# Optimization experiments

Measured on AMD Instinct MI355X. Metric: run time of the kernel, lower is better.

## Reference

```python
import jax, jax.numpy as jnp
import numpy as np

B, D, T, H = 2048, 512, 16, 1024   # batch, covariate_dim, treatment_dim, mlp hidden
K, M = 50, 16                       # k_neighbors, manifold_dim


def _mlp(xt, W1, b1, W2, b2):
    # outcome model: [B, D+T] -> [B, 1]
    return jnp.tanh(xt @ W1 + b1) @ W2 + b2


def setup_inputs() -> dict:
    key = jax.random.key(0)
    k0, k1, k2, k3, k4 = jax.random.split(key, 5)
    x = jax.random.normal(k0, (B, D), dtype=jnp.float32)
    t = jax.random.normal(k1, (B, T), dtype=jnp.float32)
    perturbations = jax.random.normal(k2, (B, D), dtype=jnp.float32)
    W1 = jax.random.normal(k3, (D + T, H), dtype=jnp.float32) / np.float32(np.sqrt(D + T))
    b1 = jnp.zeros((H,), dtype=jnp.float32)
    W2 = jax.random.normal(k4, (H, 1), dtype=jnp.float32) / np.float32(np.sqrt(H))
    b2 = jnp.zeros((1,), dtype=jnp.float32)
    return {"x": x, "t": t, "perturbations": perturbations,
            "W1": W1, "b1": b1, "W2": W2, "b2": b2}


def reference(x, t, perturbations, W1, b1, W2, b2):
    # grad of sum(y) w.r.t. x (create_graph analog handled by composing jax.grad)
    def scalar_out(xx):
        return _mlp(jnp.concatenate([xx, t], axis=-1), W1, b1, W2, b2).sum()
    grad_x = jax.grad(scalar_out)(x)                      # [B, D]

    # kNN on perturbations (squared distances preserve topk-smallest ordering)
    sq = jnp.sum(perturbations * perturbations, axis=-1)  # [B]
    d2 = sq[:, None] + sq[None, :] - 2.0 * (perturbations @ perturbations.T)
    _, idx = jax.lax.top_k(-d2, K)                        # [B, K] nearest (incl. self)

    neigh = perturbations[idx]                            # [B, K, D] gather
    centered = neigh - neigh.mean(axis=1, keepdims=True)
    # batched reduced SVD: Vt has shape [B, min(K,D), D]
    _, _, Vt = jnp.linalg.svd(centered, full_matrices=False)
    basis = jnp.swapaxes(Vt[:, :M, :], 1, 2)              # [B, D, M] top-M right sing. vecs

    # projection of grad onto tangent space, summed squared norm
    coef = jnp.einsum('bdm,bd->bm', basis, grad_x)        # [B, M]
    proj = jnp.einsum('bdm,bm->bd', basis, coef)          # [B, D]
    return jnp.sum(proj * proj) / B
```

## Files before the change

kernel.cpp:

```cpp
#include <hip/hip_runtime.h>
#include <math.h>
#include <float.h>

#define B_ 2048
#define D_ 512
#define T_ 16
#define H_ 1024
#define K_ 50
#define M_ 16
#define NSWEEP 1
#define SX_STRIDE 2656
#define SLAB 128
#define SROW 136
#define FS 52

typedef __attribute__((ext_vector_type(8))) short s16x8;
typedef __attribute__((ext_vector_type(4))) float f32x4;

__device__ __forceinline__ float bsum64(float v) {
  #pragma unroll
  for (int o = 1; o < 64; o <<= 1) v += __shfl_xor(v, o);
  return v;
}

__device__ __forceinline__ unsigned bf16_rne(float v) {
  union { float f; unsigned u; } a; a.f = v;
  return (a.u + 0x7FFFu + ((a.u >> 16) & 1u)) >> 16;
}
__device__ __forceinline__ float bf16_val(unsigned h) {
  union { unsigned u; float f; } a; a.u = h << 16;
  return a.f;
}
__device__ __forceinline__ void split_bf16(float v, unsigned short* h, unsigned short* l) {
  unsigned hh = bf16_rne(v);
  *h = (unsigned short)hh;
  *l = (unsigned short)bf16_rne(v - bf16_val(hh));
}

__global__ __launch_bounds__(256)
void prep_rows(const float* __restrict__ x, const float* __restrict__ t,
               const float* __restrict__ P,
               unsigned short* __restrict__ xh, unsigned short* __restrict__ xl,
               unsigned short* __restrict__ ph, unsigned short* __restrict__ pl,
               float* __restrict__ sq) {
  const int b = blockIdx.x, tid = threadIdx.x;
  for (int c = tid; c < 544; c += 256) {
    float v = 0.f;
    if (c < 512) v = x[(size_t)b * 512 + c];
    else if (c < 528) v = t[(size_t)b * 16 + (c - 512)];
    unsigned short hh, ll; split_bf16(v, &hh, &ll);
    xh[(size_t)b * 544 + c] = hh;
    xl[(size_t)b * 544 + c] = ll;
  }
  float s = 0.f;
  for (int c = tid; c < 512; c += 256) {
    float v = P[(size_t)b * 512 + c];
    s += v * v;
    unsigned short hh, ll; split_bf16(v, &hh, &ll);
    ph[(size_t)b * 512 + c] = hh;
    pl[(size_t)b * 512 + c] = ll;
  }
  __shared__ float red[4];
  s = bsum64(s);
  if ((tid & 63) == 0) red[tid >> 6] = s;
  __syncthreads();
  if (tid == 0) sq[b] = (red[0] + red[1]) + (red[2] + red[3]);
}

__global__ __launch_bounds__(256)
void conv_w1(const float* __restrict__ W1,
             unsigned short* __restrict__ th, unsigned short* __restrict__ tl,
             unsigned short* __restrict__ wh, unsigned short* __restrict__ wl) {
  __shared__ float tile[32][33];
  const int tx = threadIdx.x & 31, ty = threadIdx.x >> 5;
  const int kb = blockIdx.x * 32, hb = blockIdx.y * 32;
  #pragma unroll
  for (int j = 0; j < 4; j++) {
    int k = kb + ty + j * 8;
    float v = (k < 528) ? W1[(size_t)k * 1024 + hb + tx] : 0.f;
    tile[ty + j * 8][tx] = v;
    if (k < 528) {
      unsigned short hh, ll; split_bf16(v, &hh, &ll);
      wh[(size_t)k * 1024 + hb + tx] = hh;
      wl[(size_t)k * 1024 + hb + tx] = ll;
    }
  }
  __syncthreads();
  #pragma unroll
  for (int j = 0; j < 4; j++) {
    int hrow = hb + ty + j * 8;
    float v = tile[tx][ty + j * 8];
    unsigned short hh, ll; split_bf16(v, &hh, &ll);
    th[(size_t)hrow * 544 + kb + tx] = hh;
    tl[(size_t)hrow * 544 + kb + tx] = ll;
  }
}

template <int EPI, int PASSES>
__global__ __launch_bounds__(256)
void mfma_nt(const unsigned short* __restrict__ Ah, const unsigned short* __restrict__ Al, int lda,
             const unsigned short* __restrict__ Bh, const unsigned short* __restrict__ Bl, int ldb,
             int K, float* __restrict__ C, int ldc,
             const float* __restrict__ b1, const float* __restrict__ W2,
             unsigned short* __restrict__ acth, unsigned short* __restrict__ actl) {
  __shared__ unsigned short sAh[64 * 40], sBh[64 * 40];
  __shared__ unsigned short sAl[PASSES == 3 ? 64 * 40 : 16];
  __shared__ unsigned short sBl[PASSES == 3 ? 64 * 40 : 16];
  const int tid = threadIdx.x;
  const int lane = tid & 63, wv = tid >> 6;
  const int wm = wv >> 1, wn = wv & 1;
  const int lr = lane & 15, lq = lane >> 4;
  const int m0 = blockIdx.y * 64, n0 = blockIdx.x * 64;
  const int srow = tid >> 2, sk = (tid & 3) * 8;
  f32x4 acc[2][2];
  #pragma unroll
  for (int mt = 0; mt < 2; mt++)
    #pragma unroll
    for (int nt = 0; nt < 2; nt++)
      #pragma unroll
      for (int i = 0; i < 4; i++) acc[mt][nt][i] = 0.f;

  for (int kb = 0; kb < K; kb += 32) {
    float4 va = *(const float4*)(Ah + (size_t)(m0 + srow) * lda + kb + sk);
    float4 vc = *(const float4*)(Bh + (size_t)(n0 + srow) * ldb + kb + sk);
    float4 vb, vd;
    if (PASSES == 3) {
      vb = *(const float4*)(Al + (size_t)(m0 + srow) * lda + kb + sk);
      vd = *(const float4*)(Bl + (size_t)(n0 + srow) * ldb + kb + sk);
    }
    __syncthreads();
    *(float4*)&sAh[srow * 40 + sk] = va;
    *(float4*)&sBh[srow * 40 + sk] = vc;
    if (PASSES == 3) {
      *(float4*)&sAl[srow * 40 + sk] = vb;
      *(float4*)&sBl[srow * 40 + sk] = vd;
    }
    __syncthreads();
    s16x8 fah[2], fal[2], fbh[2], fbl[2];
    #pragma unroll
    for (int mt = 0; mt < 2; mt++) {
      const int r = wm * 32 + mt * 16 + lr;
      fah[mt] = *(const s16x8*)&sAh[r * 40 + lq * 8];
      if (PASSES == 3) fal[mt] = *(const s16x8*)&sAl[r * 40 + lq * 8];
    }
    #pragma unroll
    for (int nt = 0; nt < 2; nt++) {
      const int r = wn * 32 + nt * 16 + lr;
      fbh[nt] = *(const s16x8*)&sBh[r * 40 + lq * 8];
      if (PASSES == 3) fbl[nt] = *(const s16x8*)&sBl[r * 40 + lq * 8];
    }
    #pragma unroll
    for (int mt = 0; mt < 2; mt++)
      #pragma unroll
      for (int nt = 0; nt < 2; nt++)
        acc[mt][nt] = __builtin_amdgcn_mfma_f32_16x16x32_bf16(fah[mt], fbh[nt], acc[mt][nt], 0, 0, 0);
    if (PASSES == 3) {
      #pragma unroll
      for (int mt = 0; mt < 2; mt++)
        #pragma unroll
        for (int nt = 0; nt < 2; nt++)
          acc[mt][nt] = __builtin_amdgcn_mfma_f32_16x16x32_bf16(fah[mt], fbl[nt], acc[mt][nt], 0, 0, 0);
      #pragma unroll
      for (int mt = 0; mt < 2; mt++)
        #pragma unroll
        for (int nt = 0; nt < 2; nt++)
          acc[mt][nt] = __builtin_amdgcn_mfma_f32_16x16x32_bf16(fal[mt], fbh[nt], acc[mt][nt], 0, 0, 0);
    }
  }

  #pragma unroll
  for (int nt = 0; nt < 2; nt++) {
    const int n = n0 + wn * 32 + nt * 16 + lr;
    float bb = 0.f, ww = 0.f;
    if (EPI == 1) { bb = b1[n]; ww = W2[n]; }
    #pragma unroll
    for (int mt = 0; mt < 2; mt++) {
      #pragma unroll
      for (int r = 0; r < 4; r++) {
        const int m = m0 + wm * 32 + mt * 16 + lq * 4 + r;
        float v = acc[mt][nt][r];
        if (EPI == 0) {
          C[(size_t)m * ldc + n] = v;
        } else if (EPI == 1) {
          float z = v + bb;
          float e = __builtin_amdgcn_exp2f(fabsf(z) * -2.885390082f);
          float rc = __builtin_amdgcn_rcpf(1.f + e);
          float s = 4.f * e * rc * rc * ww;
          unsigned short hh, ll; split_bf16(s, &hh, &ll);
          acth[(size_t)m * ldc + n] = hh;
          actl[(size_t)m * ldc + n] = ll;
        } else {
          unsigned short hh, ll; split_bf16(v, &hh, &ll);
          acth[(size_t)m * ldc + n] = hh;
          actl[(size_t)m * ldc + n] = ll;
        }
      }
    }
  }
}

__global__ __launch_bounds__(256)
void sbuild_kernel(const unsigned short* __restrict__ ph, const unsigned short* __restrict__ pl,
                   const unsigned short* __restrict__ gh, const unsigned short* __restrict__ gl,
                   const int* __restrict__ idx, float* __restrict__ Sx) {
  __shared__ unsigned short sh[64 * SROW];
  __shared__ unsigned short sl[64 * SROW];
  __shared__ int ids[K_];
  const int b = blockIdx.x;
  const int tid = threadIdx.x;
  if (tid < K_) ids[tid] = idx[b * K_ + tid];
  const int lane = tid & 63, wv = tid >> 6;
  const int wm = wv >> 1, wn = wv & 1;
  const int lr = lane & 15, lq = lane >> 4;
  const int strow = tid >> 4, stk = (tid & 15) * 8;
  __syncthreads();

  f32x4 acc[2][2];
  #pragma unroll
  for (int mt = 0; mt < 2; mt++)
    #pragma unroll
    for (int nt = 0; nt < 2; nt++)
      #pragma unroll
      for (int i = 0; i < 4; i++) acc[mt][nt][i] = 0.f;

  for (int kb = 0; kb < 512; kb += SLAB) {
    __syncthreads();
    #pragma unroll
    for (int p = 0; p < 4; p++) {
      const int r = p * 16 + strow;
      if (r < 51) {
        const unsigned short* srch = (r < 50) ? ph + (size_t)ids[r] * 512 : gh + (size_t)b * 512;
        const unsigned short* srcl = (r < 50) ? pl + (size_t)ids[r] * 512 : gl + (size_t)b * 512;
        *(float4*)&sh[r * SROW + stk] = *(const float4*)(srch + kb + stk);
        *(float4*)&sl[r * SROW + stk] = *(const float4*)(srcl + kb + stk);
      }
    }
    __syncthreads();
    #pragma unroll
    for (int kk = 0; kk < SLAB; kk += 32) {
      s16x8 fah[2], fal[2], fbh[2], fbl[2];
      #pragma unroll
      for (int mt = 0; mt < 2; mt++) {
        const int r = wm * 32 + mt * 16 + lr;
        fah[mt] = *(const s16x8*)&sh[r * SROW + kk + lq * 8];
        fal[mt] = *(const s16x8*)&sl[r * SROW + kk + lq * 8];
      }
      #pragma unroll
      for (int nt = 0; nt < 2; nt++) {
        const int r = wn * 32 + nt * 16 + lr;
        fbh[nt] = *(const s16x8*)&sh[r * SROW + kk + lq * 8];
        fbl[nt] = *(const s16x8*)&sl[r * SROW + kk + lq * 8];
      }
      #pragma unroll
      for (int mt = 0; mt < 2; mt++)
        #pragma unroll
        for (int nt = 0; nt < 2; nt++)
          acc[mt][nt] = __builtin_amdgcn_mfma_f32_16x16x32_bf16(fah[mt], fbh[nt], acc[mt][nt], 0, 0, 0);
      #pragma unroll
      for (int mt = 0; mt < 2; mt++)
        #pragma unroll
        for (int nt = 0; nt < 2; nt++)
          acc[mt][nt] = __builtin_amdgcn_mfma_f32_16x16x32_bf16(fah[mt], fbl[nt], acc[mt][nt], 0, 0, 0);
      #pragma unroll
      for (int mt = 0; mt < 2; mt++)
        #pragma unroll
        for (int nt = 0; nt < 2; nt++)
          acc[mt][nt] = __builtin_amdgcn_mfma_f32_16x16x32_bf16(fal[mt], fbh[nt], acc[mt][nt], 0, 0, 0);
    }
  }

  float* Sb = Sx + (size_t)b * SX_STRIDE;
  #pragma unroll
  for (int nt = 0; nt < 2; nt++) {
    const int n = wn * 32 + nt * 16 + lr;
    #pragma unroll
    for (int mt = 0; mt < 2; mt++) {
      #pragma unroll
      for (int r = 0; r < 4; r++) {
        const int m = wm * 32 + mt * 16 + lq * 4 + r;
        if (m < 51 && n < 52) Sb[m * 52 + n] = acc[mt][nt][r];
      }
    }
  }
}

__device__ __forceinline__ unsigned fkey(float f) {
  unsigned u = __float_as_uint(f);
  return u ^ ((unsigned)((int)u >> 31) | 0x80000000u);
}

__global__ __launch_bounds__(64)
void topk_kernel(const float* __restrict__ G, const float* __restrict__ sq,
                 int* __restrict__ idx) {
  const int b = blockIdx.x, lane = threadIdx.x;
  const float* row = G + (size_t)b * 2048;
  unsigned k[32];
  #pragma unroll
  for (int i = 0; i < 32; i++) {
    const int j = i * 64 + lane;
    k[i] = fkey(sq[j] - 2.f * row[j]);
  }
  unsigned V = 0;
  bool exact = false;
  for (int bit = 31; bit >= 0; bit--) {
    const unsigned cand = V | (1u << bit);
    int cnt = 0;
    #pragma unroll
    for (int i = 0; i < 32; i++) cnt += (k[i] < cand) ? 1 : 0;
    #pragma unroll
    for (int o = 1; o < 64; o <<= 1) cnt += __shfl_xor(cnt, o);
    if (cnt == K_) { V = cand; exact = true; break; }
    if (cnt < K_ + 1) V = cand;
  }
  int base = 0;
  #pragma unroll
  for (int i = 0; i < 32; i++) {
    const bool p = (k[i] < V);
    const unsigned long long mask = __ballot(p);
    if (p) {
      const int pos = base + __popcll(mask & ((1ull << lane) - 1ull));
      idx[b * K_ + pos] = i * 64 + lane;
    }
    base += __popcll(mask);
  }
  if (!exact && base < K_) {
    #pragma unroll
    for (int i = 0; i < 32; i++) {
      if (base >= K_) break;
      const bool p = (k[i] == V);
      const unsigned long long mask = __ballot(p);
      if (p) {
        const int pos = base + __popcll(mask & ((1ull << lane) - 1ull));
        if (pos < K_) idx[b * K_ + pos] = i * 64 + lane;
      }
      base += __popcll(mask);
    }
  }
}

__global__ __launch_bounds__(64, 2)
void final_kernel(const float* __restrict__ Sx, float* __restrict__ out) {
  __shared__ float cols[64 * FS];
  const int b = blockIdx.x;
  const int lane = threadIdx.x;
  const float* Sb = Sx + (size_t)b * SX_STRIDE;

  float q = (lane < K_) ? Sb[50 * 52 + lane] : 0.f;
  float qm = bsum64(q) * (1.f / K_);
  float w = (lane < K_) ? (q - qm) : 0.f;

  float f[K_];
  #pragma unroll
  for (int r = 0; r < K_; r++)
    f[r] = (lane < K_) ? Sb[r * 52 + lane] : 0.f;

  float cm = 0.f;
  #pragma unroll
  for (int r = 0; r < K_; r++) cm += f[r];
  cm *= (1.f / K_);
  float gs = bsum64(lane < K_ ? cm : 0.f) * (1.f / K_);
  float cs = cm - gs;
  #pragma unroll
  for (int r = 0; r < K_; r++) {
    float rm = __shfl(cm, r);
    if (lane < K_) f[r] -= rm + cs;
  }

  float nrm = 0.f;
  #pragma unroll
  for (int r = 0; r < K_; r++) nrm += f[r] * f[r];

  float* my = &cols[lane * FS];
  #pragma unroll
  for (int k = 0; k < 12; k++) {
    float4 t = {f[4 * k], f[4 * k + 1], f[4 * k + 2], f[4 * k + 3]};
    *(float4*)&my[4 * k] = t;
  }
  {
    float4 t = {f[48], f[49], nrm, w};
    *(float4*)&my[48] = t;
  }

  for (int sweep = 0; sweep < NSWEEP; sweep++) {
    for (int r = 0; r < 49; r++) {
      const int kk = (25 * r) % 49;
      int m;
      if (lane >= K_)      m = lane;
      else if (lane == 49) m = kk;
      else if (lane == kk) m = 49;
      else { m = (r - lane) % 49; if (m < 0) m += 49; }

      const float* pc = &cols[m * FS];
      float y[52];
      #pragma unroll
      for (int k = 0; k < 13; k++) {
        float4 t = *(const float4*)&pc[4 * k];
        y[4 * k] = t.x; y[4 * k + 1] = t.y; y[4 * k + 2] = t.z; y[4 * k + 3] = t.w;
      }
      float onrm = y[50];
      float yw   = y[51];

      float d0 = 0.f, d1 = 0.f, d2 = 0.f, d3 = 0.f;
      #pragma unroll
      for (int r2 = 0; r2 < 48; r2 += 4) {
        d0 += f[r2] * y[r2];
        d1 += f[r2 + 1] * y[r2 + 1];
        d2 += f[r2 + 2] * y[r2 + 2];
        d3 += f[r2 + 3] * y[r2 + 3];
      }
      d0 += f[48] * y[48];
      d1 += f[49] * y[49];
      float dot = (d0 + d1) + (d2 + d3);

      const bool isp = lane < m;
      float alpha = isp ? nrm : onrm;
      float beta  = isp ? onrm : nrm;
      float tau = (beta - alpha) * 0.5f * __builtin_amdgcn_rcpf(dot);
      float sg = (tau >= 0.f) ? 1.f : -1.f;
      float s1 = __builtin_amdgcn_sqrtf(1.f + tau * tau);
      float tt = sg * __builtin_amdgcn_rcpf(fabsf(tau) + s1);
      float cc = __builtin_amdgcn_rsqf(1.f + tt * tt);
      float ssv = tt * cc;
      float sr = isp ? -ssv : ssv;
      if (lane >= K_ || fabsf(dot) < 1e-20f) { cc = 1.f; sr = 0.f; }
      #pragma unroll
      for (int r2 = 0; r2 < K_; r2++) f[r2] = cc * f[r2] + sr * y[r2];
      w = cc * w + sr * yw;
      nrm = cc * cc * nrm + sr * sr * onrm + 2.f * cc * sr * dot;

      #pragma unroll
      for (int k = 0; k < 12; k++) {
        float4 t = {f[4 * k], f[4 * k + 1], f[4 * k + 2], f[4 * k + 3]};
        *(float4*)&my[4 * k] = t;
      }
      float4 t = {f[48], f[49], nrm, w};
      *(float4*)&my[48] = t;
    }
  }

  float n2 = 0.f;
  #pragma unroll
  for (int r2 = 0; r2 < K_; r2++) n2 += f[r2] * f[r2];
  int rank = 0;
  #pragma unroll
  for (int j = 0; j < K_; j++) {
    float vj = __shfl(n2, j);
    rank += (vj > n2 || (vj == n2 && j < lane)) ? 1 : 0;
  }
  float lam = sqrtf(n2);
  float contrib = (lane < K_ && rank < M_) ? (w * w / lam) : 0.f;
  contrib = bsum64(contrib);
  if (lane == 0) atomicAdd(out, contrib * (1.f / B_));
}

extern "C" void kernel_launch(void* const* d_in, const int* in_sizes, int n_in,
                              void* d_out, int out_size, void* d_ws, size_t ws_size,
                              hipStream_t stream) {
  const float* x  = (const float*)d_in[0];
  const float* t  = (const float*)d_in[1];
  const float* P  = (const float*)d_in[2];
  const float* W1 = (const float*)d_in[3];
  const float* b1 = (const float*)d_in[4];
  const float* W2 = (const float*)d_in[5];
  float* out = (float*)d_out;

  float* G    = (float*)d_ws;
  float* Sx   = (float*)d_ws;
  unsigned short* xt_h  = (unsigned short*)(G + (size_t)B_ * B_);
  unsigned short* xt_l  = xt_h  + (size_t)B_ * 544;
  unsigned short* w1t_h = xt_l  + (size_t)B_ * 544;
  unsigned short* w1t_l = w1t_h + (size_t)H_ * 544;
  unsigned short* w1_h  = w1t_l + (size_t)H_ * 544;
  unsigned short* w1_l  = w1_h  + (size_t)528 * H_;
  unsigned short* p_h   = w1_l  + (size_t)528 * H_;
  unsigned short* p_l   = p_h   + (size_t)B_ * D_;
  unsigned short* act_h = p_l   + (size_t)B_ * D_;
  unsigned short* act_l = act_h + (size_t)B_ * H_;
  unsigned short* g_h   = act_l + (size_t)B_ * H_;
  unsigned short* g_l   = g_h   + (size_t)B_ * D_;
  float* sq   = (float*)(g_l + (size_t)B_ * D_);
  int*   idx  = (int*)(sq + B_);

  hipMemsetAsync(d_out, 0, sizeof(float), stream);

  prep_rows<<<B_, 256, 0, stream>>>(x, t, P, xt_h, xt_l, p_h, p_l, sq);
  conv_w1<<<dim3(17, 32), 256, 0, stream>>>(W1, w1t_h, w1t_l, w1_h, w1_l);

  mfma_nt<1, 3><<<dim3(H_ / 64, B_ / 64), 256, 0, stream>>>(
      xt_h, xt_l, 544, w1t_h, w1t_l, 544, 544,
      nullptr, H_, b1, W2, act_h, act_l);
  mfma_nt<2, 3><<<dim3(D_ / 64, B_ / 64), 256, 0, stream>>>(
      act_h, act_l, H_, w1_h, w1_l, H_, H_,
      nullptr, D_, nullptr, nullptr, g_h, g_l);
  mfma_nt<0, 1><<<dim3(B_ / 64, B_ / 64), 256, 0, stream>>>(
      p_h, nullptr, D_, p_h, nullptr, D_, D_,
      G, B_, nullptr, nullptr, nullptr, nullptr);

  topk_kernel<<<B_, 64, 0, stream>>>(G, sq, idx);
  sbuild_kernel<<<B_, 256, 0, stream>>>(p_h, p_l, g_h, g_l, idx, Sx);
  final_kernel<<<B_, 64, 0, stream>>>(Sx, out);
}
```

Measured before the change: 257.9 us.

## Split-K the grad GEMM across two slices and sort top-k indices by distance

The second GEMM (activations times W1) is now split along K into two halves via blockIdx.z. Each half writes fp32 partials to workspace, and a new reduce kernel sums them and splits the result into bf16 hi/lo. This doubles the block count from 256 to 512 so more compute units are busy, at the cost of an extra kernel launch and an fp32 round trip through memory. The top-k kernel also now ranks the selected neighbours by key and index before writing, giving a deterministic sorted order for later stages at a small extra cost per row.

```diff
diff --git a/kernel.cpp b/kernel.cpp
--- a/kernel.cpp
+++ b/kernel.cpp
@@ -106,6 +106,12 @@
   __shared__ unsigned short sAh[64 * 40], sBh[64 * 40];
   __shared__ unsigned short sAl[PASSES == 3 ? 64 * 40 : 16];
   __shared__ unsigned short sBl[PASSES == 3 ? 64 * 40 : 16];
+  if (EPI == 3) {
+    const size_t ko = (size_t)blockIdx.z * K;
+    Ah += ko; Bh += ko;
+    if (PASSES == 3) { Al += ko; Bl += ko; }
+    C += (size_t)blockIdx.z * (size_t)(gridDim.y * 64) * ldc;
+  }
   const int tid = threadIdx.x;
   const int lane = tid & 63, wv = tid >> 6;
   const int wm = wv >> 1, wn = wv & 1;
@@ -179,7 +185,7 @@
       for (int r = 0; r < 4; r++) {
         const int m = m0 + wm * 32 + mt * 16 + lq * 4 + r;
         float v = acc[mt][nt][r];
-        if (EPI == 0) {
+        if (EPI == 0 || EPI == 3) {
           C[(size_t)m * ldc + n] = v;
         } else if (EPI == 1) {
           float z = v + bb;
@@ -197,6 +203,15 @@
       }
     }
   }
+}
+
+__global__ __launch_bounds__(256)
+void grad_reduce(const float* __restrict__ Cp,
+                 unsigned short* __restrict__ gh, unsigned short* __restrict__ gl) {
+  const int i = blockIdx.x * 256 + threadIdx.x;
+  float v = Cp[i] + Cp[(size_t)B_ * D_ + i];
+  unsigned short hh, ll; split_bf16(v, &hh, &ll);
+  gh[i] = hh; gl[i] = ll;
 }
 
 __global__ __launch_bounds__(256)
@@ -292,6 +307,8 @@
 __global__ __launch_bounds__(64)
 void topk_kernel(const float* __restrict__ G, const float* __restrict__ sq,
                  int* __restrict__ idx) {
+  __shared__ unsigned skey[K_];
+  __shared__ int sidx[K_];
   const int b = blockIdx.x, lane = threadIdx.x;
   const float* row = G + (size_t)b * 2048;
   unsigned k[32];
@@ -319,7 +336,8 @@
     const unsigned long long mask = __ballot(p);
     if (p) {
       const int pos = base + __popcll(mask & ((1ull << lane) - 1ull));
-      idx[b * K_ + pos] = i * 64 + lane;
+      skey[pos] = k[i];
+      sidx[pos] = i * 64 + lane;
     }
     base += __popcll(mask);
   }
@@ -331,11 +349,22 @@
       const unsigned long long mask = __ballot(p);
       if (p) {
         const int pos = base + __popcll(mask & ((1ull << lane) - 1ull));
-        if (pos < K_) idx[b * K_ + pos] = i * 64 + lane;
+        if (pos < K_) { skey[pos] = k[i]; sidx[pos] = i * 64 + lane; }
       }
       base += __popcll(mask);
     }
   }
+  __syncthreads();
+  unsigned kp = (lane < K_) ? skey[lane] : 0xFFFFFFFFu;
+  int ip = (lane < K_) ? sidx[lane] : 0x7FFFFFFF;
+  int rank = 0;
+  #pragma unroll
+  for (int j = 0; j < K_; j++) {
+    unsigned kj = __shfl(kp, j);
+    int ij = __shfl(ip, j);
+    rank += (kj < kp || (kj == kp && ij < ip)) ? 1 : 0;
+  }
+  if (lane < K_) idx[b * K_ + rank] = ip;
 }
 
 __global__ __launch_bounds__(64, 2)
@@ -465,6 +494,7 @@
   float* out = (float*)d_out;
 
   float* G    = (float*)d_ws;
+  float* Cp   = (float*)d_ws;
   float* Sx   = (float*)d_ws;
   unsigned short* xt_h  = (unsigned short*)(G + (size_t)B_ * B_);
   unsigned short* xt_l  = xt_h  + (size_t)B_ * 544;
@@ -489,9 +519,10 @@
   mfma_nt<1, 3><<<dim3(H_ / 64, B_ / 64), 256, 0, stream>>>(
       xt_h, xt_l, 544, w1t_h, w1t_l, 544, 544,
       nullptr, H_, b1, W2, act_h, act_l);
-  mfma_nt<2, 3><<<dim3(D_ / 64, B_ / 64), 256, 0, stream>>>(
-      act_h, act_l, H_, w1_h, w1_l, H_, H_,
-      nullptr, D_, nullptr, nullptr, g_h, g_l);
+  mfma_nt<3, 3><<<dim3(D_ / 64, B_ / 64, 2), 256, 0, stream>>>(
+      act_h, act_l, H_, w1_h, w1_l, H_, 512,
+      Cp, D_, nullptr, nullptr, nullptr, nullptr);
+  grad_reduce<<<(B_ * D_) / 256, 256, 0, stream>>>(Cp, g_h, g_l);
   mfma_nt<0, 1><<<dim3(B_ / 64, B_ / 64), 256, 0, stream>>>(
       p_h, nullptr, D_, p_h, nullptr, D_, D_,
       G, B_, nullptr, nullptr, nullptr, nullptr);
```

Result: no change. 262.7 us (+1.9%).
